# Performance work log

Hardware: AMD Instinct MI355X
Metric: run time of the kernel (lower is better)

## Reference

```python
import jax, jax.numpy as jnp
import numpy as np

D_PAIR = 128
NUM_HEADS = 4
LN_EPS = 1e-5


def _mha(x, w_in, b_in, w_out, b_out, num_heads):
    # x: [B, R, S, D]; attention over axis S (keys) for each query position.
    B, R, S, D = x.shape
    hd = D // num_heads
    qkv = jnp.einsum('brsd,ed->brse', x, w_in) + b_in  # [B,R,S,3D]
    q, k, v = jnp.split(qkv, 3, axis=-1)
    q = q.reshape(B, R, S, num_heads, hd)
    k = k.reshape(B, R, S, num_heads, hd)
    v = v.reshape(B, R, S, num_heads, hd)
    scores = jnp.einsum('brqhd,brkhd->brhqk', q, k) / jnp.sqrt(jnp.asarray(hd, x.dtype))
    attn = jax.nn.softmax(scores, axis=-1)
    out = jnp.einsum('brhqk,brkhd->brqhd', attn, v).reshape(B, R, S, D)
    return jnp.einsum('brsd,ed->brse', out, w_out) + b_out


def _layernorm(x, gamma, beta):
    mu = jnp.mean(x, axis=-1, keepdims=True)
    var = jnp.mean(jnp.square(x - mu), axis=-1, keepdims=True)
    return (x - mu) * jax.lax.rsqrt(var + LN_EPS) * gamma + beta


def setup_inputs() -> dict:
    key = jax.random.key(0)
    ks = jax.random.split(key, 12)
    B, L, D = 1, 256, D_PAIR
    s = 0.02
    return {
        'pair_repr': jax.random.normal(ks[0], (B, L, L, D), dtype=jnp.float32),
        'chain_id_tensor': jax.random.randint(ks[1], (L,), 0, 2),
        'w_in_s': jax.random.normal(ks[2], (3 * D, D), dtype=jnp.float32) * s,
        'b_in_s': jnp.zeros((3 * D,), jnp.float32),
        'w_out_s': jax.random.normal(ks[3], (D, D), dtype=jnp.float32) * s,
        'b_out_s': jnp.zeros((D,), jnp.float32),
        'w_in_e': jax.random.normal(ks[4], (3 * D, D), dtype=jnp.float32) * s,
        'b_in_e': jnp.zeros((3 * D,), jnp.float32),
        'w_out_e': jax.random.normal(ks[5], (D, D), dtype=jnp.float32) * s,
        'b_out_e': jnp.zeros((D,), jnp.float32),
        'gamma_s': jnp.ones((D,), jnp.float32),
        'beta_s': jnp.zeros((D,), jnp.float32),
        'gamma_e': jnp.ones((D,), jnp.float32),
        'beta_e': jnp.zeros((D,), jnp.float32),
        'w_gate': jax.random.normal(ks[6], (D, D), dtype=jnp.float32) * s,
        'b_gate': jnp.zeros((D,), jnp.float32),
    }


def reference(pair_repr, chain_id_tensor, w_in_s, b_in_s, w_out_s, b_out_s,
              w_in_e, b_in_e, w_out_e, b_out_e, gamma_s, beta_s,
              gamma_e, beta_e, w_gate, b_gate):
    # Row-wise (starting node) attention: attend over axis 2.
    attn_i = _mha(pair_repr, w_in_s, b_in_s, w_out_s, b_out_s, NUM_HEADS)
    pair = _layernorm(pair_repr + attn_i, gamma_s, beta_s)
    # Column-wise (ending node) attention: transpose rows/cols, attend, transpose back.
    pair_t = jnp.swapaxes(pair, 1, 2)
    attn_j = _mha(pair_t, w_in_e, b_in_e, w_out_e, b_out_e, NUM_HEADS)
    pair = _layernorm(pair + jnp.swapaxes(attn_j, 1, 2), gamma_e, beta_e)
    gate = jax.nn.sigmoid(jnp.einsum('bijd,ed->bije', pair, w_gate) + b_gate)
    return pair * gate
```

## Files before the change

### kernel.cpp

```cpp
#include <hip/hip_runtime.h>
#include <hip/hip_bf16.h>
#include <cstddef>

#define DD 128

typedef unsigned short u16;
typedef short short8v __attribute__((ext_vector_type(8)));
typedef float floatx4 __attribute__((ext_vector_type(4)));
typedef float floatx16 __attribute__((ext_vector_type(16)));

__device__ __forceinline__ float bf2f(u16 u) {
    return __uint_as_float(((unsigned int)u) << 16);
}
__device__ __forceinline__ u16 f2b(float x) {
    unsigned u = __float_as_uint(x);
    return (u16)((u + 0x7FFF + ((u >> 16) & 1)) >> 16);
}
__device__ __forceinline__ unsigned cvtpk_bf16(float lo, float hi) {
    unsigned r;
    asm("v_cvt_pk_bf16_f32 %0, %1, %2" : "=v"(r) : "v"(lo), "v"(hi));
    return r;
}

__global__ __launch_bounds__(512) void wcvt_kernel(
    const float* __restrict__ a0, const float* __restrict__ a1,
    const float* __restrict__ a2, const float* __restrict__ a3,
    const float* __restrict__ a4, u16* __restrict__ dst)
{
    int q = blockIdx.x * 512 + threadIdx.x;
    int i = q * 4;
    const float* src; int off;
    if      (i < 49152)  { src = a0; off = 0; }
    else if (i < 65536)  { src = a1; off = 49152; }
    else if (i < 114688) { src = a2; off = 65536; }
    else if (i < 131072) { src = a3; off = 114688; }
    else                 { src = a4; off = 131072; }
    float4 v = *reinterpret_cast<const float4*>(src + (i - off));
    ushort4 o = { f2b(v.x), f2b(v.y), f2b(v.z), f2b(v.w) };
    *reinterpret_cast<ushort4*>(dst + i) = o;
}

__device__ __forceinline__ void stage_wb(const u16* __restrict__ Wb,
                                         u16* __restrict__ Wl, int tid) {
    #pragma unroll
    for (int it = 0; it < 4; ++it) {
        int f = tid + it * 512;
        int row = f >> 4, c8 = f & 15;
        uint4 v = *reinterpret_cast<const uint4*>(Wb + (size_t)row * DD + c8 * 8);
        *reinterpret_cast<uint4*>(&Wl[row * 136 + c8 * 8]) = v;
    }
}

__global__ __launch_bounds__(512) void proj_qkv_mfma(
    const float* __restrict__ Xf, const u16* __restrict__ Xb,
    const u16* __restrict__ Wb, const float* __restrict__ bias,
    __hip_bfloat16* __restrict__ QKo, __hip_bfloat16* __restrict__ VTo)
{
    __shared__ u16 Wl[128 * 136];
    const int tid = threadIdx.x;
    const int tok0 = blockIdx.x * 128;
    const int lane = tid & 63, wq = tid >> 6;
    const int lq = lane & 15, g = lane >> 4;
    const int t = tok0 + wq * 16 + lq;

    short8v bfrag[4];
    if (Xb) {
        #pragma unroll
        for (int ks = 0; ks < 4; ++ks)
            bfrag[ks] = *reinterpret_cast<const short8v*>(Xb + (size_t)t * DD + ks * 32 + g * 8);
    } else {
        #pragma unroll
        for (int ks = 0; ks < 4; ++ks) {
            const float* p = Xf + (size_t)t * DD + ks * 32 + g * 8;
            float4 a = *reinterpret_cast<const float4*>(p);
            float4 b = *reinterpret_cast<const float4*>(p + 4);
            u16 tmp[8] = { f2b(a.x), f2b(a.y), f2b(a.z), f2b(a.w),
                           f2b(b.x), f2b(b.y), f2b(b.z), f2b(b.w) };
            bfrag[ks] = *reinterpret_cast<const short8v*>(tmp);
        }
    }

    u16* qkt = reinterpret_cast<u16*>(QKo) + (size_t)t * 256;
    u16* vtb = reinterpret_cast<u16*>(VTo);
    const int rr_ = t >> 8, kk_ = t & 255;

    for (int c = 0; c < 3; ++c) {
        if (c) __syncthreads();
        stage_wb(Wb + (size_t)c * 128 * DD, Wl, tid);
        __syncthreads();
        #pragma unroll
        for (int et = 0; et < 8; ++et) {
            float4 b4 = *reinterpret_cast<const float4*>(bias + c * 128 + et * 16 + g * 4);
            floatx4 acc = { b4.x, b4.y, b4.z, b4.w };
            #pragma unroll
            for (int ks = 0; ks < 4; ++ks) {
                short8v afrag = *reinterpret_cast<const short8v*>(
                    &Wl[(et * 16 + lq) * 136 + ks * 32 + g * 8]);
                acc = __builtin_amdgcn_mfma_f32_16x16x32_bf16(afrag, bfrag[ks], acc, 0, 0, 0);
            }
            if (c < 2) {
                ushort4 o;
                o.x = f2b(acc[0]); o.y = f2b(acc[1]); o.z = f2b(acc[2]); o.w = f2b(acc[3]);
                *reinterpret_cast<ushort4*>(&qkt[c * 128 + et * 16 + g * 4]) = o;
            } else {
                int e = et * 16 + g * 4;
                int hh = e >> 5, dbase = e & 31;
                u16* vb = vtb + ((size_t)(rr_ * 4 + hh) * 32 + dbase) * 256 + kk_;
                vb[0]   = f2b(acc[0]);
                vb[256] = f2b(acc[1]);
                vb[512] = f2b(acc[2]);
                vb[768] = f2b(acc[3]);
            }
        }
    }
}

__global__ __launch_bounds__(512, 4) void attn_mfma_kernel(
    const __hip_bfloat16* __restrict__ QK, const __hip_bfloat16* __restrict__ VT,
    __hip_bfloat16* __restrict__ O, int swap_store)
{
    constexpr int KP = 40;
    constexpr int VP = 264;
    __shared__ u16 K_lds[256 * KP];
    __shared__ u16 Vt_lds[32 * VP];

    const int tid = threadIdx.x;
    const int bid = blockIdx.x;
    const int xcd = bid & 7, m = bid >> 3;
    const int r = xcd * 32 + (m >> 2);
    const int h = m & 3;
    const u16* qk = reinterpret_cast<const u16*>(QK) + (size_t)r * 65536;
    const u16* vt = reinterpret_cast<const u16*>(VT) + ((size_t)r * 4 + h) * 8192;

    #pragma unroll
    for (int it = 0; it < 2; ++it) {
        int f = tid + it * 512;
        int row = f >> 2, c = f & 3;
        uint4 v = *reinterpret_cast<const uint4*>(qk + (size_t)row * 256 + 128 + h * 32 + c * 8);
        *reinterpret_cast<uint4*>(&K_lds[row * KP + c * 8]) = v;
    }
    #pragma unroll
    for (int it = 0; it < 2; ++it) {
        int f = tid + it * 512;
        int row = f >> 5, c = f & 31;
        uint4 v = *reinterpret_cast<const uint4*>(vt + row * 256 + c * 8);
        *reinterpret_cast<uint4*>(&Vt_lds[row * VP + c * 8]) = v;
    }
    __syncthreads();

    const int lane = tid & 63;
    const int wq = tid >> 6;
    const int ql = lane & 31;
    const int hi = lane >> 5;
    const int q0 = wq * 32;
    const float C1 = 0.25505654196988f;

    short8v qf0 = *reinterpret_cast<const short8v*>(
        qk + (size_t)(q0 + ql) * 256 + h * 32 + hi * 8);
    short8v qf1 = *reinterpret_cast<const short8v*>(
        qk + (size_t)(q0 + ql) * 256 + h * 32 + 16 + hi * 8);

    const floatx16 zf = {0.f,0.f,0.f,0.f,0.f,0.f,0.f,0.f,
                         0.f,0.f,0.f,0.f,0.f,0.f,0.f,0.f};

    floatx16 acc = zf;
    float ell = 0.f;

    __builtin_amdgcn_s_setprio(1);
    #pragma unroll
    for (int b = 0; b < 8; ++b) {
        short8v k0 = *reinterpret_cast<const short8v*>(&K_lds[(32 * b + ql) * KP + hi * 8]);
        short8v k1 = *reinterpret_cast<const short8v*>(&K_lds[(32 * b + ql) * KP + 16 + hi * 8]);
        floatx16 s = zf;
        s = __builtin_amdgcn_mfma_f32_32x32x16_bf16(k0, qf0, s, 0, 0, 0);
        s = __builtin_amdgcn_mfma_f32_32x32x16_bf16(k1, qf1, s, 0, 0, 0);

        unsigned u[8];
        #pragma unroll
        for (int e = 0; e < 4; ++e) {
            float p0 = __builtin_amdgcn_exp2f(s[4*e+0] * C1);
            float p1 = __builtin_amdgcn_exp2f(s[4*e+1] * C1);
            float p2 = __builtin_amdgcn_exp2f(s[4*e+2] * C1);
            float p3 = __builtin_amdgcn_exp2f(s[4*e+3] * C1);
            ell += (p0 + p1) + (p2 + p3);
            u[2*e]     = cvtpk_bf16(p0, p1);
            u[2*e + 1] = cvtpk_bf16(p2, p3);
        }

        #pragma unroll
        for (int be = 0; be < 2; ++be) {
            const int kb = 2 * b + be;
            int a0 = (int)u[4*be + 2], b0 = (int)u[4*be + 0];
            asm("v_permlane32_swap_b32 %0, %1" : "+v"(a0), "+v"(b0));
            int a1 = (int)u[4*be + 3], b1 = (int)u[4*be + 1];
            asm("v_permlane32_swap_b32 %0, %1" : "+v"(a1), "+v"(b1));
            union { int i[4]; short8v v; } pu;
            pu.i[0] = b0; pu.i[1] = b1; pu.i[2] = a0; pu.i[3] = a1;
            short8v vf = *reinterpret_cast<const short8v*>(&Vt_lds[ql * VP + kb * 16 + hi * 8]);
            acc = __builtin_amdgcn_mfma_f32_32x32x16_bf16(vf, pu.v, acc, 0, 0, 0);
        }
    }
    __builtin_amdgcn_s_setprio(0);

    {
        float ex = ell, ey = ell;
        asm("v_permlane32_swap_b32 %0, %1" : "+v"(ex), "+v"(ey));
        ell = ex + ey;
    }

    const float inv = 1.f / ell;
    const int q = q0 + ql;
    const size_t opos = swap_store ? ((size_t)q * 256 + r) : ((size_t)r * 256 + q);
    u16* ob = reinterpret_cast<u16*>(O) + (size_t)h * 2097152 + opos * 32;
    #pragma unroll
    for (int e = 0; e < 4; ++e) {
        ushort4 w = { f2b(acc[4*e+0] * inv), f2b(acc[4*e+1] * inv),
                      f2b(acc[4*e+2] * inv), f2b(acc[4*e+3] * inv) };
        *reinterpret_cast<ushort4*>(ob + e * 8 + hi * 4) = w;
    }
}

__global__ __launch_bounds__(512) void proj_ln_mfma(
    const __hip_bfloat16* __restrict__ A, const u16* __restrict__ Wb,
    const float* __restrict__ bias, const float* __restrict__ RES,
    const float* __restrict__ gamma, const float* __restrict__ beta,
    u16* __restrict__ RESb, u16* __restrict__ Xt)
{
    __shared__ u16 Wl[128 * 136];
    const int tid = threadIdx.x;
    const int tok0 = blockIdx.x * 128;
    const int lane = tid & 63, wq = tid >> 6;
    const int lq = lane & 15, g = lane >> 4;
    const int t = tok0 + wq * 16 + lq;
    const u16* A16 = reinterpret_cast<const u16*>(A);

    stage_wb(Wb, Wl, tid);

    short8v bfrag[4];
    #pragma unroll
    for (int ks = 0; ks < 4; ++ks)
        bfrag[ks] = *reinterpret_cast<const short8v*>(
            A16 + (size_t)ks * 2097152 + (size_t)t * 32 + g * 8);

    __syncthreads();

    floatx4 acc[8];
    #pragma unroll
    for (int et = 0; et < 8; ++et) {
        float4 b4 = *reinterpret_cast<const float4*>(bias + et * 16 + g * 4);
        float4 r4 = *reinterpret_cast<const float4*>(RES + (size_t)t * DD + et * 16 + g * 4);
        acc[et] = { b4.x + r4.x, b4.y + r4.y, b4.z + r4.z, b4.w + r4.w };
        #pragma unroll
        for (int ks = 0; ks < 4; ++ks) {
            short8v afrag = *reinterpret_cast<const short8v*>(
                &Wl[(et * 16 + lq) * 136 + ks * 32 + g * 8]);
            acc[et] = __builtin_amdgcn_mfma_f32_16x16x32_bf16(afrag, bfrag[ks], acc[et], 0, 0, 0);
        }
    }

    float s = 0.f, ss = 0.f;
    #pragma unroll
    for (int et = 0; et < 8; ++et)
        #pragma unroll
        for (int rr = 0; rr < 4; ++rr) { float v = acc[et][rr]; s += v; ss += v * v; }
    s  += __shfl_xor(s, 16);  s  += __shfl_xor(s, 32);
    ss += __shfl_xor(ss, 16); ss += __shfl_xor(ss, 32);
    float mu = s * (1.f / 128.f);
    float var = ss * (1.f / 128.f) - mu * mu;
    float rstd = rsqrtf(var + 1e-5f);

    u16* xt = Xt + (size_t)((t & 255) * 256 + (t >> 8)) * DD;
    u16* rb = RESb + (size_t)t * DD;
    #pragma unroll
    for (int et = 0; et < 8; ++et) {
        float4 g4 = *reinterpret_cast<const float4*>(gamma + et * 16 + g * 4);
        float4 be4 = *reinterpret_cast<const float4*>(beta + et * 16 + g * 4);
        float4 o4;
        o4.x = (acc[et][0] - mu) * rstd * g4.x + be4.x;
        o4.y = (acc[et][1] - mu) * rstd * g4.y + be4.y;
        o4.z = (acc[et][2] - mu) * rstd * g4.z + be4.z;
        o4.w = (acc[et][3] - mu) * rstd * g4.w + be4.w;
        ushort4 xb = { f2b(o4.x), f2b(o4.y), f2b(o4.z), f2b(o4.w) };
        *reinterpret_cast<ushort4*>(&xt[et * 16 + g * 4]) = xb;
        *reinterpret_cast<ushort4*>(&rb[et * 16 + g * 4]) = xb;
    }
}

__global__ __launch_bounds__(512) void proj_ln_gate_mfma(
    const __hip_bfloat16* __restrict__ A, const u16* __restrict__ Wb,
    const float* __restrict__ bias, const u16* __restrict__ RESb,
    const float* __restrict__ gamma, const float* __restrict__ beta,
    const u16* __restrict__ Wgb, const float* __restrict__ bg,
    float* __restrict__ OUT)
{
    __shared__ u16 Wl[128 * 136];
    __shared__ u16 Yl[128 * 136];
    const int tid = threadIdx.x;
    const int tok0 = blockIdx.x * 128;
    const int lane = tid & 63, wq = tid >> 6;
    const int lq = lane & 15, g = lane >> 4;
    const int tl = wq * 16 + lq;
    const int t = tok0 + tl;
    const u16* A16 = reinterpret_cast<const u16*>(A);

    stage_wb(Wb, Wl, tid);

    short8v bfrag[4];
    #pragma unroll
    for (int ks = 0; ks < 4; ++ks)
        bfrag[ks] = *reinterpret_cast<const short8v*>(
            A16 + (size_t)ks * 2097152 + (size_t)t * 32 + g * 8);

    __syncthreads();

    floatx4 acc[8];
    #pragma unroll
    for (int et = 0; et < 8; ++et) {
        float4 b4 = *reinterpret_cast<const float4*>(bias + et * 16 + g * 4);
        ushort4 rv = *reinterpret_cast<const ushort4*>(RESb + (size_t)t * DD + et * 16 + g * 4);
        acc[et] = { b4.x + bf2f(rv.x), b4.y + bf2f(rv.y),
                    b4.z + bf2f(rv.z), b4.w + bf2f(rv.w) };
        #pragma unroll
        for (int ks = 0; ks < 4; ++ks) {
            short8v afrag = *reinterpret_cast<const short8v*>(
                &Wl[(et * 16 + lq) * 136 + ks * 32 + g * 8]);
            acc[et] = __builtin_amdgcn_mfma_f32_16x16x32_bf16(afrag, bfrag[ks], acc[et], 0, 0, 0);
        }
    }

    float s = 0.f, ss = 0.f;
    #pragma unroll
    for (int et = 0; et < 8; ++et)
        #pragma unroll
        for (int rr = 0; rr < 4; ++rr) { float v = acc[et][rr]; s += v; ss += v * v; }
    s  += __shfl_xor(s, 16);  s  += __shfl_xor(s, 32);
    ss += __shfl_xor(ss, 16); ss += __shfl_xor(ss, 32);
    float mu = s * (1.f / 128.f);
    float var = ss * (1.f / 128.f) - mu * mu;
    float rstd = rsqrtf(var + 1e-5f);

    #pragma unroll
    for (int et = 0; et < 8; ++et) {
        float4 g4 = *reinterpret_cast<const float4*>(gamma + et * 16 + g * 4);
        float4 be4 = *reinterpret_cast<const float4*>(beta + et * 16 + g * 4);
        acc[et][0] = (acc[et][0] - mu) * rstd * g4.x + be4.x;
        acc[et][1] = (acc[et][1] - mu) * rstd * g4.y + be4.y;
        acc[et][2] = (acc[et][2] - mu) * rstd * g4.z + be4.z;
        acc[et][3] = (acc[et][3] - mu) * rstd * g4.w + be4.w;
        ushort4 yb;
        yb.x = f2b(acc[et][0]); yb.y = f2b(acc[et][1]);
        yb.z = f2b(acc[et][2]); yb.w = f2b(acc[et][3]);
        *reinterpret_cast<ushort4*>(&Yl[tl * 136 + et * 16 + g * 4]) = yb;
    }

    __syncthreads();
    stage_wb(Wgb, Wl, tid);
    __syncthreads();

    short8v yfrag[4];
    #pragma unroll
    for (int ks = 0; ks < 4; ++ks)
        yfrag[ks] = *reinterpret_cast<const short8v*>(&Yl[tl * 136 + ks * 32 + g * 8]);

    #pragma unroll
    for (int et = 0; et < 8; ++et) {
        float4 b4 = *reinterpret_cast<const float4*>(bg + et * 16 + g * 4);
        floatx4 z = { b4.x, b4.y, b4.z, b4.w };
        #pragma unroll
        for (int ks = 0; ks < 4; ++ks) {
            short8v afrag = *reinterpret_cast<const short8v*>(
                &Wl[(et * 16 + lq) * 136 + ks * 32 + g * 8]);
            z = __builtin_amdgcn_mfma_f32_16x16x32_bf16(afrag, yfrag[ks], z, 0, 0, 0);
        }
        float4 o4;
        o4.x = acc[et][0] / (1.f + __expf(-z[0]));
        o4.y = acc[et][1] / (1.f + __expf(-z[1]));
        o4.z = acc[et][2] / (1.f + __expf(-z[2]));
        o4.w = acc[et][3] / (1.f + __expf(-z[3]));
        *reinterpret_cast<float4*>(OUT + (size_t)t * DD + et * 16 + g * 4) = o4;
    }
}

extern "C" void kernel_launch(void* const* d_in, const int* in_sizes, int n_in,
                              void* d_out, int out_size, void* d_ws, size_t ws_size,
                              hipStream_t stream) {
    const float* pair    = (const float*)d_in[0];
    const float* w_in_s  = (const float*)d_in[2];
    const float* b_in_s  = (const float*)d_in[3];
    const float* w_out_s = (const float*)d_in[4];
    const float* b_out_s = (const float*)d_in[5];
    const float* w_in_e  = (const float*)d_in[6];
    const float* b_in_e  = (const float*)d_in[7];
    const float* w_out_e = (const float*)d_in[8];
    const float* b_out_e = (const float*)d_in[9];
    const float* gamma_s = (const float*)d_in[10];
    const float* beta_s  = (const float*)d_in[11];
    const float* gamma_e = (const float*)d_in[12];
    const float* beta_e  = (const float*)d_in[13];
    const float* w_gate  = (const float*)d_in[14];
    const float* b_gate  = (const float*)d_in[15];
    float* out = (float*)d_out;

    __hip_bfloat16* qk   = (__hip_bfloat16*)d_ws;
    __hip_bfloat16* vt   = qk + (size_t)65536 * 256;
    __hip_bfloat16* attn = vt + (size_t)1024 * 32 * 256;
    u16*            xt   = (u16*)(attn + (size_t)65536 * 128);
    u16*            resb = xt + (size_t)65536 * 128;
    u16*            wb   = resb + (size_t)65536 * 128;

    wcvt_kernel<<<80, 512, 0, stream>>>(w_in_s, w_out_s, w_in_e, w_out_e, w_gate, wb);

    proj_qkv_mfma<<<512, 512, 0, stream>>>(pair, nullptr, wb, b_in_s, qk, vt);
    attn_mfma_kernel<<<1024, 512, 0, stream>>>(qk, vt, attn, 0);
    proj_ln_mfma<<<512, 512, 0, stream>>>(attn, wb + 49152, b_out_s, pair,
                                          gamma_s, beta_s, resb, xt);
    proj_qkv_mfma<<<512, 512, 0, stream>>>(nullptr, xt, wb + 65536, b_in_e, qk, vt);
    attn_mfma_kernel<<<1024, 512, 0, stream>>>(qk, vt, attn, 1);
    proj_ln_gate_mfma<<<512, 512, 0, stream>>>(attn, wb + 114688, b_out_e, resb,
                                               gamma_e, beta_e, wb + 131072, b_gate,
                                               out);
}
```

Measured before the change: 132.2 us.

## Fuse QKV projection into attention kernel, dropping QK/VT global round trip

Merges the QKV projection kernel into the attention kernel. Each block (one row, one head) stages the row's 256 tokens of input into LDS, computes its head's Q, K and V with 32x32 MFMAs, and writes K and V^T straight into LDS for attention. This removes the global write and re-read of the QK and VT intermediates and one launch per attention stage. In exchange, each row's input is loaded and projected by four head blocks instead of once, the weights are read directly from global memory, and register and LDS pressure rise under the 4-blocks-per-CU launch bound.

```diff
diff --git a/kernel.cpp b/kernel.cpp
--- a/kernel.cpp
+++ b/kernel.cpp
@@ -20,6 +20,25 @@
     unsigned r;
     asm("v_cvt_pk_bf16_f32 %0, %1, %2" : "=v"(r) : "v"(lo), "v"(hi));
     return r;
+}
+
+__device__ __forceinline__ void repack16(const floatx16& a, short8v& f0, short8v& f1) {
+    unsigned u[8];
+    #pragma unroll
+    for (int e = 0; e < 4; ++e) {
+        u[2*e]   = cvtpk_bf16(a[4*e+0], a[4*e+1]);
+        u[2*e+1] = cvtpk_bf16(a[4*e+2], a[4*e+3]);
+    }
+    #pragma unroll
+    for (int be = 0; be < 2; ++be) {
+        int a0 = (int)u[4*be+2], b0 = (int)u[4*be+0];
+        asm("v_permlane32_swap_b32 %0, %1" : "+v"(a0), "+v"(b0));
+        int a1 = (int)u[4*be+3], b1 = (int)u[4*be+1];
+        asm("v_permlane32_swap_b32 %0, %1" : "+v"(a1), "+v"(b1));
+        union { int i[4]; short8v v; } pu;
+        pu.i[0] = b0; pu.i[1] = b1; pu.i[2] = a0; pu.i[3] = a1;
+        if (be == 0) f0 = pu.v; else f1 = pu.v;
+    }
 }
 
 __global__ __launch_bounds__(512) void wcvt_kernel(
@@ -51,100 +70,42 @@
     }
 }
 
-__global__ __launch_bounds__(512) void proj_qkv_mfma(
+__global__ __launch_bounds__(512, 4) void fused_qkv_attn(
     const float* __restrict__ Xf, const u16* __restrict__ Xb,
     const u16* __restrict__ Wb, const float* __restrict__ bias,
-    __hip_bfloat16* __restrict__ QKo, __hip_bfloat16* __restrict__ VTo)
-{
-    __shared__ u16 Wl[128 * 136];
-    const int tid = threadIdx.x;
-    const int tok0 = blockIdx.x * 128;
-    const int lane = tid & 63, wq = tid >> 6;
-    const int lq = lane & 15, g = lane >> 4;
-    const int t = tok0 + wq * 16 + lq;
-
-    short8v bfrag[4];
-    if (Xb) {
-        #pragma unroll
-        for (int ks = 0; ks < 4; ++ks)
-            bfrag[ks] = *reinterpret_cast<const short8v*>(Xb + (size_t)t * DD + ks * 32 + g * 8);
-    } else {
-        #pragma unroll
-        for (int ks = 0; ks < 4; ++ks) {
-            const float* p = Xf + (size_t)t * DD + ks * 32 + g * 8;
-            float4 a = *reinterpret_cast<const float4*>(p);
-            float4 b = *reinterpret_cast<const float4*>(p + 4);
-            u16 tmp[8] = { f2b(a.x), f2b(a.y), f2b(a.z), f2b(a.w),
-                           f2b(b.x), f2b(b.y), f2b(b.z), f2b(b.w) };
-            bfrag[ks] = *reinterpret_cast<const short8v*>(tmp);
-        }
-    }
-
-    u16* qkt = reinterpret_cast<u16*>(QKo) + (size_t)t * 256;
-    u16* vtb = reinterpret_cast<u16*>(VTo);
-    const int rr_ = t >> 8, kk_ = t & 255;
-
-    for (int c = 0; c < 3; ++c) {
-        if (c) __syncthreads();
-        stage_wb(Wb + (size_t)c * 128 * DD, Wl, tid);
-        __syncthreads();
-        #pragma unroll
-        for (int et = 0; et < 8; ++et) {
-            float4 b4 = *reinterpret_cast<const float4*>(bias + c * 128 + et * 16 + g * 4);
-            floatx4 acc = { b4.x, b4.y, b4.z, b4.w };
-            #pragma unroll
-            for (int ks = 0; ks < 4; ++ks) {
-                short8v afrag = *reinterpret_cast<const short8v*>(
-                    &Wl[(et * 16 + lq) * 136 + ks * 32 + g * 8]);
-                acc = __builtin_amdgcn_mfma_f32_16x16x32_bf16(afrag, bfrag[ks], acc, 0, 0, 0);
-            }
-            if (c < 2) {
-                ushort4 o;
-                o.x = f2b(acc[0]); o.y = f2b(acc[1]); o.z = f2b(acc[2]); o.w = f2b(acc[3]);
-                *reinterpret_cast<ushort4*>(&qkt[c * 128 + et * 16 + g * 4]) = o;
-            } else {
-                int e = et * 16 + g * 4;
-                int hh = e >> 5, dbase = e & 31;
-                u16* vb = vtb + ((size_t)(rr_ * 4 + hh) * 32 + dbase) * 256 + kk_;
-                vb[0]   = f2b(acc[0]);
-                vb[256] = f2b(acc[1]);
-                vb[512] = f2b(acc[2]);
-                vb[768] = f2b(acc[3]);
-            }
-        }
-    }
-}
-
-__global__ __launch_bounds__(512, 4) void attn_mfma_kernel(
-    const __hip_bfloat16* __restrict__ QK, const __hip_bfloat16* __restrict__ VT,
     __hip_bfloat16* __restrict__ O, int swap_store)
 {
+    constexpr int XP = 136;
     constexpr int KP = 40;
     constexpr int VP = 264;
-    __shared__ u16 K_lds[256 * KP];
-    __shared__ u16 Vt_lds[32 * VP];
+    __shared__ u16 SMEM[256 * XP];
+    u16* X_lds  = SMEM;
+    u16* K_lds  = SMEM;
+    u16* Vt_lds = SMEM + 256 * KP;
 
     const int tid = threadIdx.x;
     const int bid = blockIdx.x;
-    const int xcd = bid & 7, m = bid >> 3;
-    const int r = xcd * 32 + (m >> 2);
-    const int h = m & 3;
-    const u16* qk = reinterpret_cast<const u16*>(QK) + (size_t)r * 65536;
-    const u16* vt = reinterpret_cast<const u16*>(VT) + ((size_t)r * 4 + h) * 8192;
-
-    #pragma unroll
-    for (int it = 0; it < 2; ++it) {
-        int f = tid + it * 512;
-        int row = f >> 2, c = f & 3;
-        uint4 v = *reinterpret_cast<const uint4*>(qk + (size_t)row * 256 + 128 + h * 32 + c * 8);
-        *reinterpret_cast<uint4*>(&K_lds[row * KP + c * 8]) = v;
-    }
-    #pragma unroll
-    for (int it = 0; it < 2; ++it) {
-        int f = tid + it * 512;
-        int row = f >> 5, c = f & 31;
-        uint4 v = *reinterpret_cast<const uint4*>(vt + row * 256 + c * 8);
-        *reinterpret_cast<uint4*>(&Vt_lds[row * VP + c * 8]) = v;
+    const int xcd = bid & 7, mm = bid >> 3;
+    const int r = xcd * 32 + (mm >> 2);
+    const int h = mm & 3;
+
+    if (Xb) {
+        const u16* xs = Xb + (size_t)r * 256 * DD;
+        #pragma unroll
+        for (int it = 0; it < 4; ++it) {
+            int f = tid + it * 512, row = f >> 4, c8 = f & 15;
+            uint4 v = *reinterpret_cast<const uint4*>(xs + row * DD + c8 * 8);
+            *reinterpret_cast<uint4*>(&X_lds[row * XP + c8 * 8]) = v;
+        }
+    } else {
+        const float* xs = Xf + (size_t)r * 256 * DD;
+        #pragma unroll
+        for (int it = 0; it < 16; ++it) {
+            int f = tid + it * 512, row = f >> 5, c4 = f & 31;
+            float4 v = *reinterpret_cast<const float4*>(xs + row * DD + c4 * 4);
+            ushort4 o = { f2b(v.x), f2b(v.y), f2b(v.z), f2b(v.w) };
+            *reinterpret_cast<ushort4*>(&X_lds[row * XP + c4 * 4]) = o;
+        }
     }
     __syncthreads();
 
@@ -152,14 +113,55 @@
     const int wq = tid >> 6;
     const int ql = lane & 31;
     const int hi = lane >> 5;
-    const int q0 = wq * 32;
+    const int t0 = wq * 32;
+
+    const u16* Wq = Wb + (size_t)(h * 32) * DD;
+    const u16* Wk = Wb + (size_t)(128 + h * 32) * DD;
+    const u16* Wv = Wb + (size_t)(256 + h * 32) * DD;
+
+    floatx16 qa, ka, va;
+    #pragma unroll
+    for (int k2 = 0; k2 < 4; ++k2) {
+        int d0 = 8 * k2 + 4 * hi;
+        float4 b1 = *reinterpret_cast<const float4*>(bias + h * 32 + d0);
+        float4 b2 = *reinterpret_cast<const float4*>(bias + 128 + h * 32 + d0);
+        float4 b3 = *reinterpret_cast<const float4*>(bias + 256 + h * 32 + d0);
+        qa[4*k2+0] = b1.x; qa[4*k2+1] = b1.y; qa[4*k2+2] = b1.z; qa[4*k2+3] = b1.w;
+        ka[4*k2+0] = b2.x; ka[4*k2+1] = b2.y; ka[4*k2+2] = b2.z; ka[4*k2+3] = b2.w;
+        va[4*k2+0] = b3.x; va[4*k2+1] = b3.y; va[4*k2+2] = b3.z; va[4*k2+3] = b3.w;
+    }
+
+    #pragma unroll
+    for (int ks = 0; ks < 8; ++ks) {
+        short8v xb = *reinterpret_cast<const short8v*>(
+            &X_lds[(t0 + ql) * XP + ks * 16 + hi * 8]);
+        short8v aq = *reinterpret_cast<const short8v*>(Wq + (size_t)ql * DD + ks * 16 + hi * 8);
+        short8v ak = *reinterpret_cast<const short8v*>(Wk + (size_t)ql * DD + ks * 16 + hi * 8);
+        short8v av = *reinterpret_cast<const short8v*>(Wv + (size_t)ql * DD + ks * 16 + hi * 8);
+        qa = __builtin_amdgcn_mfma_f32_32x32x16_bf16(aq, xb, qa, 0, 0, 0);
+        ka = __builtin_amdgcn_mfma_f32_32x32x16_bf16(ak, xb, ka, 0, 0, 0);
+        va = __builtin_amdgcn_mfma_f32_32x32x16_bf16(av, xb, va, 0, 0, 0);
+    }
+
+    short8v qf0, qf1, kf0, kf1;
+    repack16(qa, qf0, qf1);
+    repack16(ka, kf0, kf1);
+    u16 vb16[16];
+    #pragma unroll
+    for (int rr = 0; rr < 16; ++rr) vb16[rr] = f2b(va[rr]);
+
+    __syncthreads();
+
+    *reinterpret_cast<uint4*>(&K_lds[(t0 + ql) * KP + hi * 8]) =
+        *reinterpret_cast<const uint4*>(&kf0);
+    *reinterpret_cast<uint4*>(&K_lds[(t0 + ql) * KP + 16 + hi * 8]) =
+        *reinterpret_cast<const uint4*>(&kf1);
+    #pragma unroll
+    for (int rr = 0; rr < 16; ++rr)
+        Vt_lds[((rr & 3) + 8 * (rr >> 2) + 4 * hi) * VP + t0 + ql] = vb16[rr];
+    __syncthreads();
+
     const float C1 = 0.25505654196988f;
-
-    short8v qf0 = *reinterpret_cast<const short8v*>(
-        qk + (size_t)(q0 + ql) * 256 + h * 32 + hi * 8);
-    short8v qf1 = *reinterpret_cast<const short8v*>(
-        qk + (size_t)(q0 + ql) * 256 + h * 32 + 16 + hi * 8);
-
     const floatx16 zf = {0.f,0.f,0.f,0.f,0.f,0.f,0.f,0.f,
                          0.f,0.f,0.f,0.f,0.f,0.f,0.f,0.f};
 
@@ -209,7 +211,7 @@
     }
 
     const float inv = 1.f / ell;
-    const int q = q0 + ql;
+    const int q = t0 + ql;
     const size_t opos = swap_store ? ((size_t)q * 256 + r) : ((size_t)r * 256 + q);
     u16* ob = reinterpret_cast<u16*>(O) + (size_t)h * 2097152 + opos * 32;
     #pragma unroll
@@ -401,21 +403,17 @@
     const float* b_gate  = (const float*)d_in[15];
     float* out = (float*)d_out;
 
-    __hip_bfloat16* qk   = (__hip_bfloat16*)d_ws;
-    __hip_bfloat16* vt   = qk + (size_t)65536 * 256;
-    __hip_bfloat16* attn = vt + (size_t)1024 * 32 * 256;
+    __hip_bfloat16* attn = (__hip_bfloat16*)d_ws;
     u16*            xt   = (u16*)(attn + (size_t)65536 * 128);
     u16*            resb = xt + (size_t)65536 * 128;
     u16*            wb   = resb + (size_t)65536 * 128;
 
     wcvt_kernel<<<80, 512, 0, stream>>>(w_in_s, w_out_s, w_in_e, w_out_e, w_gate, wb);
 
-    proj_qkv_mfma<<<512, 512, 0, stream>>>(pair, nullptr, wb, b_in_s, qk, vt);
-    attn_mfma_kernel<<<1024, 512, 0, stream>>>(qk, vt, attn, 0);
+    fused_qkv_attn<<<1024, 512, 0, stream>>>(pair, nullptr, wb, b_in_s, attn, 0);
     proj_ln_mfma<<<512, 512, 0, stream>>>(attn, wb + 49152, b_out_s, pair,
                                           gamma_s, beta_s, resb, xt);
-    proj_qkv_mfma<<<512, 512, 0, stream>>>(nullptr, xt, wb + 65536, b_in_e, qk, vt);
-    attn_mfma_kernel<<<1024, 512, 0, stream>>>(qk, vt, attn, 1);
+    fused_qkv_attn<<<1024, 512, 0, stream>>>(nullptr, xt, wb + 65536, b_in_e, attn, 1);
     proj_ln_gate_mfma<<<512, 512, 0, stream>>>(attn, wb + 114688, b_out_e, resb,
                                                gamma_e, beta_e, wb + 131072, b_gate,
                                                out);
```

New measurement: 126.4 us. 4.4% less time.
